# Kernel optimization log

Measured on AMD Instinct MI355X. Metric: run time of the kernel, lower is better.

## Reference

```python
import jax, jax.numpy as jnp
import numpy as np

N_QUBITS = 8
N_CYCLES = 4
N_LAYERS = 2  # log2(8) - 1
B = 65536

CNOT = jnp.array([[1, 0, 0, 0],
                  [0, 1, 0, 0],
                  [0, 0, 0, 1],
                  [0, 0, 1, 0]], dtype=jnp.complex64)


def apply_gate(state, U, wires):
    """Apply a (2^k x 2^k) gate U on the given wires of state (B, 2,2,...,2).
    Wire 0 is the leftmost (most significant) qubit axis."""
    k = len(wires)
    src = [w + 1 for w in wires]
    dst = list(range(1, 1 + k))
    st = jnp.moveaxis(state, src, dst)
    shp = st.shape
    st = st.reshape(shp[0], 2 ** k, -1)
    st = jnp.einsum('ij,bjr->bir', U, st)
    return jnp.moveaxis(st.reshape(shp), dst, src)


def apply_ry(state, q, angles):
    """Batched RY(angle) on qubit q; angles has shape (B,)."""
    st = jnp.moveaxis(state, q + 1, 1)  # (B, 2, rest...)
    c = jnp.cos(0.5 * angles).reshape((-1,) + (1,) * (st.ndim - 2))
    s = jnp.sin(0.5 * angles).reshape((-1,) + (1,) * (st.ndim - 2))
    s0, s1 = st[:, 0], st[:, 1]
    new = jnp.stack([c * s0 - s * s1, s * s0 + c * s1], axis=1)
    return jnp.moveaxis(new, 1, q + 1)


def crx_mat(theta):
    c = (jnp.cos(0.5 * theta) + 0j).astype(jnp.complex64)
    s = (-1j * jnp.sin(0.5 * theta)).astype(jnp.complex64)
    one = jnp.ones((), jnp.complex64)
    zero = jnp.zeros((), jnp.complex64)
    return jnp.stack([
        jnp.stack([one, zero, zero, zero]),
        jnp.stack([zero, one, zero, zero]),
        jnp.stack([zero, zero, c, s]),
        jnp.stack([zero, zero, s, c]),
    ])


def u3_mat(p):
    th, ph, lm = p[0], p[1], p[2]
    ct = (jnp.cos(0.5 * th) + 0j).astype(jnp.complex64)
    st = (jnp.sin(0.5 * th) + 0j).astype(jnp.complex64)
    el = jnp.exp(1j * lm).astype(jnp.complex64)
    ep = jnp.exp(1j * ph).astype(jnp.complex64)
    return jnp.stack([
        jnp.stack([ct, -el * st]),
        jnp.stack([ep * st, ep * el * ct]),
    ])


def expval_z(state, q):
    st = jnp.moveaxis(state, q + 1, 1)
    p = (st.real ** 2 + st.imag ** 2).reshape(st.shape[0], 2, -1).sum(-1)
    return p[:, 0] - p[:, 1]


def _forward(x, crx_theta, u3_params, w1, b1, w2, b2):
    b = x.shape[0]
    # |0...0> initial state, shape (B, 2,2,...,2)
    state = jnp.zeros((b, 2 ** N_QUBITS), jnp.complex64).at[:, 0].set(1.0)
    state = state.reshape((b,) + (2,) * N_QUBITS)
    # encoder: data re-uploading RY angle encoding + CNOT ring, n_cycles times
    for _ in range(N_CYCLES):
        for q in range(N_QUBITS):
            state = apply_ry(state, q, x[:, q])
        for q in range(N_QUBITS):
            state = apply_gate(state, CNOT, [q, (q + 1) % N_QUBITS])
    # QCNN conv/pool layers with shared weights per layer
    active = list(range(N_QUBITS))
    for layer in range(N_LAYERS):
        U = crx_mat(crx_theta[layer])
        for i in range(0, len(active) - 1, 2):
            state = apply_gate(state, U, [active[i], active[i + 1]])
        for i in range(1, len(active) - 1, 2):
            state = apply_gate(state, U, [active[i], active[i + 1]])
        remain = active[1::2]
        # mid-circuit expval in the original is discarded and does not alter state
        V = u3_mat(u3_params[layer])
        for q in remain:
            state = apply_gate(state, V, [q])
        active = remain
    feats = jnp.stack([expval_z(state, q) for q in active], axis=1)  # (B, 2)
    h = jnp.tanh(feats @ w1 + b1)
    return jax.nn.sigmoid(h @ w2 + b2)  # (B, 1)


def setup_inputs() -> dict:
    key = jax.random.key(0)
    ks = jax.random.split(key, 6)
    return {
        'x': jax.random.normal(ks[0], (B, N_QUBITS), jnp.float32),
        'crx_theta': jax.random.normal(ks[1], (N_LAYERS,), jnp.float32),
        'u3_params': jax.random.normal(ks[2], (N_LAYERS, 3), jnp.float32),
        'w1': jax.random.normal(ks[3], (2, 10), jnp.float32) * 0.5,
        'b1': jnp.zeros((10,), jnp.float32),
        'w2': jax.random.normal(ks[4], (10, 1), jnp.float32) * 0.5,
        'b2': jnp.zeros((1,), jnp.float32),
    }


def reference(x, crx_theta, u3_params, w1, b1, w2, b2):
    return _forward(x, crx_theta, u3_params, w1, b1, w2, b2)
```

## Files before the change

kernel.cpp:

```cpp
#include <hip/hip_runtime.h>


#define NQ 8
typedef _Float16 h2 __attribute__((ext_vector_type(2)));

__device__ __forceinline__ float h2f(h2 v){ return __builtin_bit_cast(float, v); }
__device__ __forceinline__ h2 f2h(float v){ return __builtin_bit_cast(h2, v); }
__device__ __forceinline__ h2 u2h(unsigned u){ return __builtin_bit_cast(h2, u); }
__device__ __forceinline__ h2 negh(h2 v){ return __builtin_bit_cast(h2, __builtin_bit_cast(unsigned, v) ^ 0x80008000u); }
__device__ __forceinline__ h2 mk(float x){ _Float16 h=(_Float16)x; return (h2){h,h}; }
__device__ __forceinline__ h2 mk2(float a, float b){ return (h2){(_Float16)a,(_Float16)b}; }
__device__ __forceinline__ h2 fma2h(h2 a, h2 b, h2 c){ return __builtin_elementwise_fma(a,b,c); }
__device__ __forceinline__ h2 swp(h2 v){ return __builtin_shufflevector(v,v,1,0); }

template<int CTRL>
__device__ __forceinline__ float dppf(float v){
    return __int_as_float(__builtin_amdgcn_mov_dpp(__float_as_int(v), CTRL, 0xF, 0xF, true));
}
template<int M>
__device__ __forceinline__ float sx(float v){
    if constexpr (M==1)       return dppf<0xB1>(v);
    else if constexpr (M==2)  return dppf<0x4E>(v);
    else if constexpr (M==8)  return dppf<0x128>(v);
    else if constexpr (M==32) return __shfl_xor(v, 32, 64);
    else return __int_as_float(__builtin_amdgcn_ds_swizzle(__float_as_int(v), (M<<10)|0x1F));
}
__device__ __forceinline__ float bperm(int ba, float v){
    return __int_as_float(__builtin_amdgcn_ds_bpermute(ba, __float_as_int(v)));
}
__device__ __forceinline__ void cmulh(h2&R, h2&I, h2 C, h2 S, h2 nS){
    h2 nR = fma2h(C, R, nS*I);
    I = fma2h(C, I, S*R);
    R = nR;
}

__global__ void qcnn_prep(const float* __restrict__ crx,
                          const float* __restrict__ u3p,
                          unsigned* __restrict__ ws){
    if (threadIdx.x==0 && blockIdx.x==0){
        auto PK=[](float lo, float hi)->unsigned{
            unsigned a=__builtin_bit_cast(unsigned short,(_Float16)lo);
            unsigned b=__builtin_bit_cast(unsigned short,(_Float16)hi);
            return a | (b<<16);
        };
        float sc0,cc0,sc1,cc1;
        __sincosf(0.5f*crx[0],&sc0,&cc0);
        __sincosf(0.5f*crx[1],&sc1,&cc1);
        ws[0]=PK(cc0,cc0); ws[1]=PK(sc0,sc0); ws[2]=PK(cc1,cc1); ws[3]=PK(sc1,sc1);
        float th0=u3p[0], ph0=u3p[1], lm0=u3p[2];
        float ust0,uct0; __sincosf(0.5f*th0,&ust0,&uct0);
        ws[4]=PK(uct0,uct0); ws[5]=PK(ust0,ust0); ws[6]=PK(-ust0,-ust0); ws[7]=PK(-ust0,ust0);
        float th1=u3p[3], ph1=u3p[4], lm1=u3p[5];
        float ust1,uct1; __sincosf(0.5f*th1,&ust1,&uct1);
        float sl1,cl1;   __sincosf(lm1,&sl1,&cl1);
        float sp1,cp1;   __sincosf(ph1,&sp1,&cp1);
        ws[8]=PK(uct1,uct1); ws[9]=PK(ust1,ust1); ws[10]=PK(-ust1,-ust1);
        ws[11]=PK(cl1,cl1); ws[12]=PK(sl1,sl1); ws[13]=PK(cp1,cp1); ws[14]=PK(sp1,sp1);
        float cpl1=cp1*cl1-sp1*sl1, spl1=sp1*cl1+cp1*sl1;
        float u01r=-ust1*cl1, u01i=-ust1*sl1;
        float u10r= ust1*cp1, u10i= ust1*sp1;
        float u11r= uct1*cpl1, u11i= uct1*spl1;
        ws[15]=PK(uct1,u11r); ws[16]=PK(u01r,u10r); ws[17]=PK(0.f,-u11i);
        ws[18]=PK(-u01i,-u10i); ws[19]=PK(0.f,u11i); ws[20]=PK(u01i,u10i);
        for(int k=0;k<4;++k){
            float kf=(float)k, sA,cA,sB,cB,sA2,cA2,sB2,cB2;
            __sincosf(lm0*kf,      &sA,&cA);
            __sincosf(lm0*(kf+1.f),&sB,&cB);
            __sincosf(ph0*kf,      &sA2,&cA2);
            __sincosf(ph0*(kf+1.f),&sB2,&cB2);
            unsigned* q = ws + 24 + k*4;
            q[0]=PK(cA,cB); q[1]=PK(sA,sB); q[2]=PK(cA2,cB2); q[3]=PK(sA2,sB2);
        }
    }
}

__global__ __launch_bounds__(256) void qcnn_kernel(
    const float* __restrict__ x,
    const unsigned* __restrict__ wsu,
    const float* __restrict__ w1,
    const float* __restrict__ b1,
    const float* __restrict__ w2,
    const float* __restrict__ b2,
    float* __restrict__ out,
    int Btot)
{
    const int gtid = blockIdx.x*256 + threadIdx.x;
    const int e = gtid >> 6;
    const int l = threadIdx.x & 63;
    if (e >= Btot) return;
    const bool L5=(l>>5)&1, L4=(l>>4)&1, L3=(l>>3)&1, L2=(l>>2)&1, L1=(l>>1)&1, L0=l&1;

    const bool pb = __builtin_popcount(l) & 1;
    const int ba0 = (((l&32)|((l^(l>>1))&31)) << 2);
    const int ba1 = ba0 ^ (48<<2);

    const float4* xv = (const float4*)(x + e*NQ);
    float4 xa=xv[0], xb=xv[1];
    float ang[8]={xa.x,xa.y,xa.z,xa.w,xb.x,xb.y,xb.z,xb.w};
    float cq[8], sq[8];
#pragma unroll
    for(int q=0;q<8;++q) __sincosf(0.5f*ang[q], &sq[q], &cq[q]);
    h2 cH[6], tsH[6];
    const bool bits[6]={L5,L4,L3,L2,L1,L0};
#pragma unroll
    for(int q=0;q<6;++q){
        cH[q]=mk(cq[q]);
        h2 sh=mk(sq[q]);
        tsH[q]= bits[q] ? sh : negh(sh);
    }
    h2 c6h=mk(cq[6]), s6h=mk(sq[6]), ns6h=negh(s6h);
    h2 c7h=mk(cq[7]), sv7h=mk2(-sq[7], sq[7]);

    const h2 cc0h=u2h(wsu[0]), sn0h=u2h(wsu[1]), cc1h=u2h(wsu[2]), sn1h=u2h(wsu[3]);
    const h2 nsn0h=negh(sn0h), nsn1h=negh(sn1h);
    const h2 uct0h=u2h(wsu[4]), ust0h=u2h(wsu[5]), nust0h=u2h(wsu[6]), usv0h=u2h(wsu[7]);
    const h2 uct1h=u2h(wsu[8]), ust1h=u2h(wsu[9]), nust1h=u2h(wsu[10]);
    const h2 cl1h=u2h(wsu[11]), sl1h=u2h(wsu[12]), nsl1h=negh(sl1h);
    const h2 cp1h=u2h(wsu[13]), sp1h=u2h(wsu[14]), nsp1h=negh(sp1h);
    const h2 E0h=u2h(wsu[15]), E1h=u2h(wsu[16]), E2h=u2h(wsu[17]);
    const h2 E3h=u2h(wsu[18]), G2h=u2h(wsu[19]), G3h=u2h(wsu[20]);
    const int ki = (int)L4 + (int)L2 + (int)L0;
    uint4 dt = *(const uint4*)(wsu + 24 + ki*4);
    const h2 Clm=u2h(dt.x), Slm=u2h(dt.y), Cph=u2h(dt.z), Sph=u2h(dt.w);
    const h2 nSlm=negh(Slm), nSph=negh(Sph);
    const h2 tu1H = L4 ? ust0h : nust0h;
    const h2 tu3H = L2 ? ust0h : nust0h;
    const h2 tu5H = L0 ? ust0h : nust0h;

    h2 A, B;
    {
        float pl = (L5?sq[0]:cq[0])*(L4?sq[1]:cq[1])*(L3?sq[2]:cq[2])
                 * (L2?sq[3]:cq[3])*(L1?sq[4]:cq[4])*(L0?sq[5]:cq[5]);
        float pc6=pl*cq[6], ps6=pl*sq[6];
        A = mk2(pc6*cq[7], pc6*sq[7]);
        B = mk2(ps6*cq[7], ps6*sq[7]);
    }

#define RY_L(q, M) do { \
    h2 oA = f2h(sx<M>(h2f(A))), oB = f2h(sx<M>(h2f(B))); \
    A = fma2h(cH[q], A, tsH[q]*oA); \
    B = fma2h(cH[q], B, tsH[q]*oB); \
} while(0)

#define RINGF() do { \
    float TA = h2f(pb ? B : A); \
    float TS = h2f(swp(pb ? A : B)); \
    float u0 = bperm(ba0, TA), u1 = bperm(ba1, TA); \
    float w0 = bperm(ba0, TS), w1 = bperm(ba1, TS); \
    A = (h2){ f2h(u0).x, f2h(u1).y }; \
    B = (h2){ f2h(w0).x, f2h(w1).y }; \
} while(0)

    RINGF();
#pragma unroll
    for(int cyc=0;cyc<3;++cyc){
        RY_L(0,32); RY_L(1,16); RY_L(2,8); RY_L(3,4); RY_L(4,2); RY_L(5,1);
        { h2 nA = fma2h(c6h, A, ns6h*B);
          h2 nB = fma2h(s6h, A, c6h*B);
          A=nA; B=nB; }
        A = fma2h(c7h, A, sv7h*swp(A));
        B = fma2h(c7h, B, sv7h*swp(B));
        RINGF();
    }

    h2 RA=A, RB=B, IA=(h2){0,0}, IB=(h2){0,0};

#define SHF4(M) h2 oRA=f2h(sx<M>(h2f(RA))), oIA=f2h(sx<M>(h2f(IA))), \
                   oRB=f2h(sx<M>(h2f(RB))), oIB=f2h(sx<M>(h2f(IB)));
#define CRX_LL(CSH, M, cc, sn, nsn) do { \
    const bool ct = (l >> (CSH)) & 1; \
    SHF4(M) \
    if (ct) { \
        RA = fma2h(cc, RA, (sn)*oIA); IA = fma2h(cc, IA, (nsn)*oRA); \
        RB = fma2h(cc, RB, (sn)*oIB); IB = fma2h(cc, IB, (nsn)*oRB); } \
} while(0)
#define RYC0(M, T) do { \
    SHF4(M) \
    RA = fma2h(uct0h, RA, (T)*oRA); IA = fma2h(uct0h, IA, (T)*oIA); \
    RB = fma2h(uct0h, RB, (T)*oRB); IB = fma2h(uct0h, IB, (T)*oIB); \
} while(0)

    {   h2 oA = f2h(sx<16>(h2f(RA))), oB = f2h(sx<16>(h2f(RB)));
        if (L5){ IA = nsn0h*oA; RA = cc0h*RA; IB = nsn0h*oB; RB = cc0h*RB; }
    }
    CRX_LL(3, 4, cc0h, sn0h, nsn0h);
    CRX_LL(1, 1, cc0h, sn0h, nsn0h);
    {   h2 oI = swp(IB), oR = swp(RB);
        RB = fma2h(cc0h, RB, sn0h*oI);
        IB = fma2h(cc0h, IB, nsn0h*oR);
    }
    CRX_LL(4, 8, cc0h, sn0h, nsn0h);
    CRX_LL(2, 2, cc0h, sn0h, nsn0h);
    if (L0) {
        h2 nRA = fma2h(cc0h, RA, sn0h*IB);
        h2 nRB = fma2h(cc0h, RB, sn0h*IA);
        h2 nIA = fma2h(cc0h, IA, nsn0h*RB);
        h2 nIB = fma2h(cc0h, IB, nsn0h*RA);
        RA=nRA; RB=nRB; IA=nIA; IB=nIB;
    }
    cmulh(RA,IA,Clm,Slm,nSlm); cmulh(RB,IB,Clm,Slm,nSlm);
    RYC0(16, tu1H);
    RYC0(4,  tu3H);
    RYC0(1,  tu5H);
    {   h2 sA=swp(RA), sB=swp(RB), tA=swp(IA), tB=swp(IB);
        RA = fma2h(uct0h, RA, usv0h*sA); RB = fma2h(uct0h, RB, usv0h*sB);
        IA = fma2h(uct0h, IA, usv0h*tA); IB = fma2h(uct0h, IB, usv0h*tB);
    }
    cmulh(RA,IA,Cph,Sph,nSph); cmulh(RB,IB,Cph,Sph,nSph);

    CRX_LL(4, 4, cc1h, sn1h, nsn1h);
    if (L0) {
        h2 sIA=swp(IA), sRA=swp(RA), sIB=swp(IB), sRB=swp(RB);
        RA = fma2h(cc1h, RA, sn1h*sIA); IA = fma2h(cc1h, IA, nsn1h*sRA);
        RB = fma2h(cc1h, RB, sn1h*sIB); IB = fma2h(cc1h, IB, nsn1h*sRB);
    }
    CRX_LL(2, 1, cc1h, sn1h, nsn1h);
    {
        if (L2){ cmulh(RA,IA,cl1h,sl1h,nsl1h); cmulh(RB,IB,cl1h,sl1h,nsl1h); }
        h2 T = L2 ? ust1h : nust1h;
        SHF4(4)
        RA = fma2h(uct1h, RA, T*oRA); IA = fma2h(uct1h, IA, T*oIA);
        RB = fma2h(uct1h, RB, T*oRB); IB = fma2h(uct1h, IB, T*oIB);
        if (L2){ cmulh(RA,IA,cp1h,sp1h,nsp1h); cmulh(RB,IB,cp1h,sp1h,nsp1h); }
    }
    {
        h2 sR=swp(RA), sI=swp(IA);
        h2 nR = fma2h(E3h,sI, fma2h(E2h,IA, fma2h(E1h,sR, E0h*RA)));
        h2 nI = fma2h(G3h,sR, fma2h(G2h,RA, fma2h(E1h,sI, E0h*IA)));
        RA=nR; IA=nI;
        h2 sR2=swp(RB), sI2=swp(IB);
        h2 nR2 = fma2h(E3h,sI2, fma2h(E2h,IB, fma2h(E1h,sR2, E0h*RB)));
        h2 nI2 = fma2h(G3h,sR2, fma2h(G2h,RB, fma2h(E1h,sI2, E0h*IB)));
        RB=nR2; IB=nI2;
    }

    float r0=(float)RA.x, r1=(float)RA.y, r2=(float)RB.x, r3=(float)RB.y;
    float i0=(float)IA.x, i1=(float)IA.y, i2=(float)IB.x, i3=(float)IB.y;
    float n0=fmaf(i0,i0,r0*r0), n1=fmaf(i1,i1,r1*r1);
    float n2=fmaf(i2,i2,r2*r2), n3=fmaf(i3,i3,r3*r3);
    float tot=(n0+n1)+(n2+n3);
    float f0 = L2 ? -tot : tot;
    float f1 = (n0-n1)+(n2-n3);
    f0 += sx<1>(f0);  f1 += sx<1>(f1);
    f0 += sx<2>(f0);  f1 += sx<2>(f1);
    f0 += sx<4>(f0);  f1 += sx<4>(f1);
    f0 += sx<8>(f0);  f1 += sx<8>(f1);
    f0 += sx<16>(f0); f1 += sx<16>(f1);
    f0 += sx<32>(f0); f1 += sx<32>(f1);

    const int k = l & 15;
    float contrib = 0.0f;
    if (k < 10) {
        float z = fmaf(f0, w1[k], fmaf(f1, w1[10+k], b1[k]));
        float ex = __expf(2.0f*z);
        contrib = ((ex-1.0f)/(ex+1.0f)) * w2[k];
    }
    contrib += sx<1>(contrib);
    contrib += sx<2>(contrib);
    contrib += sx<4>(contrib);
    contrib += sx<8>(contrib);
    if (l == 0) {
        float a = contrib + b2[0];
        out[e] = 1.0f/(1.0f + __expf(-a));
    }
}

extern "C" void kernel_launch(void* const* d_in, const int* in_sizes, int n_in,
                              void* d_out, int out_size, void* d_ws, size_t ws_size,
                              hipStream_t stream) {
    const float* x   = (const float*)d_in[0];
    const float* crx = (const float*)d_in[1];
    const float* u3p = (const float*)d_in[2];
    const float* w1  = (const float*)d_in[3];
    const float* b1  = (const float*)d_in[4];
    const float* w2  = (const float*)d_in[5];
    const float* b2  = (const float*)d_in[6];
    float* out = (float*)d_out;
    unsigned* ws = (unsigned*)d_ws;

    const int B = in_sizes[0] / NQ;
    hipLaunchKernelGGL(qcnn_prep, dim3(1), dim3(64), 0, stream, crx, u3p, ws);
    const int wavesPerBlock = 4;
    const int grid = (B + wavesPerBlock - 1) / wavesPerBlock;
    hipLaunchKernelGGL(qcnn_kernel, dim3(grid), dim3(256), 0, stream,
                       x, ws, w1, b1, w2, b2, out, B);
}
```

Baseline: 122.0 us.

## Process two batch elements per wavefront to amortize per-wave setup and add ILP

```diff
diff --git a/kernel.cpp b/kernel.cpp
--- a/kernel.cpp
+++ b/kernel.cpp
@@ -21,7 +21,6 @@
 __device__ __forceinline__ float sx(float v){
     if constexpr (M==1)       return dppf<0xB1>(v);
     else if constexpr (M==2)  return dppf<0x4E>(v);
-    else if constexpr (M==8)  return dppf<0x128>(v);
     else if constexpr (M==32) return __shfl_xor(v, 32, 64);
     else return __int_as_float(__builtin_amdgcn_ds_swizzle(__float_as_int(v), (M<<10)|0x1F));
 }
@@ -33,6 +32,8 @@
     I = fma2h(C, I, S*R);
     R = nR;
 }
+
+#define FOR_E _Pragma("unroll") for (int e = 0; e < 2; ++e)
 
 __global__ void qcnn_prep(const float* __restrict__ crx,
                           const float* __restrict__ u3p,
@@ -85,31 +86,41 @@
     int Btot)
 {
     const int gtid = blockIdx.x*256 + threadIdx.x;
-    const int e = gtid >> 6;
+    const int wv = gtid >> 6;
     const int l = threadIdx.x & 63;
-    if (e >= Btot) return;
+    const int e0 = wv * 2;
+    if (e0 >= Btot) return;
     const bool L5=(l>>5)&1, L4=(l>>4)&1, L3=(l>>3)&1, L2=(l>>2)&1, L1=(l>>1)&1, L0=l&1;
 
     const bool pb = __builtin_popcount(l) & 1;
     const int ba0 = (((l&32)|((l^(l>>1))&31)) << 2);
     const int ba1 = ba0 ^ (48<<2);
 
-    const float4* xv = (const float4*)(x + e*NQ);
-    float4 xa=xv[0], xb=xv[1];
-    float ang[8]={xa.x,xa.y,xa.z,xa.w,xb.x,xb.y,xb.z,xb.w};
-    float cq[8], sq[8];
+    h2 cH[2][6], tsH[2][6];
+    h2 c6h[2], s6h[2], ns6h[2], c7h[2], sv7h[2];
+    h2 A[2], B[2];
+    const bool bits[6]={L5,L4,L3,L2,L1,L0};
+    FOR_E {
+        const float4* xv = (const float4*)(x + (e0+e)*NQ);
+        float4 xa=xv[0], xb=xv[1];
+        float ang[8]={xa.x,xa.y,xa.z,xa.w,xb.x,xb.y,xb.z,xb.w};
+        float cq[8], sq[8];
 #pragma unroll
-    for(int q=0;q<8;++q) __sincosf(0.5f*ang[q], &sq[q], &cq[q]);
-    h2 cH[6], tsH[6];
-    const bool bits[6]={L5,L4,L3,L2,L1,L0};
+        for(int q=0;q<8;++q) __sincosf(0.5f*ang[q], &sq[q], &cq[q]);
 #pragma unroll
-    for(int q=0;q<6;++q){
-        cH[q]=mk(cq[q]);
-        h2 sh=mk(sq[q]);
-        tsH[q]= bits[q] ? sh : negh(sh);
-    }
-    h2 c6h=mk(cq[6]), s6h=mk(sq[6]), ns6h=negh(s6h);
-    h2 c7h=mk(cq[7]), sv7h=mk2(-sq[7], sq[7]);
+        for(int q=0;q<6;++q){
+            cH[e][q]=mk(cq[q]);
+            h2 sh=mk(sq[q]);
+            tsH[e][q]= bits[q] ? sh : negh(sh);
+        }
+        c6h[e]=mk(cq[6]); s6h[e]=mk(sq[6]); ns6h[e]=negh(s6h[e]);
+        c7h[e]=mk(cq[7]); sv7h[e]=mk2(-sq[7], sq[7]);
+        float pl = (L5?sq[0]:cq[0])*(L4?sq[1]:cq[1])*(L3?sq[2]:cq[2])
+                 * (L2?sq[3]:cq[3])*(L1?sq[4]:cq[4])*(L0?sq[5]:cq[5]);
+        float pc6=pl*cq[6], ps6=pl*sq[6];
+        A[e] = mk2(pc6*cq[7], pc6*sq[7]);
+        B[e] = mk2(ps6*cq[7], ps6*sq[7]);
+    }
 
     const h2 cc0h=u2h(wsu[0]), sn0h=u2h(wsu[1]), cc1h=u2h(wsu[2]), sn1h=u2h(wsu[3]);
     const h2 nsn0h=negh(sn0h), nsn1h=negh(sn1h);
@@ -127,131 +138,136 @@
     const h2 tu3H = L2 ? ust0h : nust0h;
     const h2 tu5H = L0 ? ust0h : nust0h;
 
-    h2 A, B;
-    {
-        float pl = (L5?sq[0]:cq[0])*(L4?sq[1]:cq[1])*(L3?sq[2]:cq[2])
-                 * (L2?sq[3]:cq[3])*(L1?sq[4]:cq[4])*(L0?sq[5]:cq[5]);
-        float pc6=pl*cq[6], ps6=pl*sq[6];
-        A = mk2(pc6*cq[7], pc6*sq[7]);
-        B = mk2(ps6*cq[7], ps6*sq[7]);
-    }
-
-#define RY_L(q, M) do { \
-    h2 oA = f2h(sx<M>(h2f(A))), oB = f2h(sx<M>(h2f(B))); \
-    A = fma2h(cH[q], A, tsH[q]*oA); \
-    B = fma2h(cH[q], B, tsH[q]*oB); \
+#define RY_L(q, M) do { FOR_E { \
+    h2 oA = f2h(sx<M>(h2f(A[e]))), oB = f2h(sx<M>(h2f(B[e]))); \
+    A[e] = fma2h(cH[e][q], A[e], tsH[e][q]*oA); \
+    B[e] = fma2h(cH[e][q], B[e], tsH[e][q]*oB); } \
 } while(0)
 
-#define RINGF() do { \
-    float TA = h2f(pb ? B : A); \
-    float TS = h2f(swp(pb ? A : B)); \
+#define RINGF() do { FOR_E { \
+    float TA = h2f(pb ? B[e] : A[e]); \
+    float TS = h2f(swp(pb ? A[e] : B[e])); \
     float u0 = bperm(ba0, TA), u1 = bperm(ba1, TA); \
     float w0 = bperm(ba0, TS), w1 = bperm(ba1, TS); \
-    A = (h2){ f2h(u0).x, f2h(u1).y }; \
-    B = (h2){ f2h(w0).x, f2h(w1).y }; \
+    A[e] = (h2){ f2h(u0).x, f2h(u1).y }; \
+    B[e] = (h2){ f2h(w0).x, f2h(w1).y }; } \
 } while(0)
 
     RINGF();
 #pragma unroll
     for(int cyc=0;cyc<3;++cyc){
         RY_L(0,32); RY_L(1,16); RY_L(2,8); RY_L(3,4); RY_L(4,2); RY_L(5,1);
-        { h2 nA = fma2h(c6h, A, ns6h*B);
-          h2 nB = fma2h(s6h, A, c6h*B);
-          A=nA; B=nB; }
-        A = fma2h(c7h, A, sv7h*swp(A));
-        B = fma2h(c7h, B, sv7h*swp(B));
+        FOR_E { h2 nA = fma2h(c6h[e], A[e], ns6h[e]*B[e]);
+                h2 nB = fma2h(s6h[e], A[e], c6h[e]*B[e]);
+                A[e]=nA; B[e]=nB; }
+        FOR_E { A[e] = fma2h(c7h[e], A[e], sv7h[e]*swp(A[e]));
+                B[e] = fma2h(c7h[e], B[e], sv7h[e]*swp(B[e])); }
         RINGF();
     }
 
-    h2 RA=A, RB=B, IA=(h2){0,0}, IB=(h2){0,0};
-
-#define SHF4(M) h2 oRA=f2h(sx<M>(h2f(RA))), oIA=f2h(sx<M>(h2f(IA))), \
-                   oRB=f2h(sx<M>(h2f(RB))), oIB=f2h(sx<M>(h2f(IB)));
+    h2 RA[2], RB[2], IA[2], IB[2];
+    FOR_E { RA[e]=A[e]; RB[e]=B[e]; IA[e]=(h2){0,0}; IB[e]=(h2){0,0}; }
+
+#define SHF4(M) h2 oRA[2], oIA[2], oRB[2], oIB[2]; \
+    FOR_E { oRA[e]=f2h(sx<M>(h2f(RA[e]))); oIA[e]=f2h(sx<M>(h2f(IA[e]))); \
+            oRB[e]=f2h(sx<M>(h2f(RB[e]))); oIB[e]=f2h(sx<M>(h2f(IB[e]))); }
 #define CRX_LL(CSH, M, cc, sn, nsn) do { \
     const bool ct = (l >> (CSH)) & 1; \
     SHF4(M) \
-    if (ct) { \
-        RA = fma2h(cc, RA, (sn)*oIA); IA = fma2h(cc, IA, (nsn)*oRA); \
-        RB = fma2h(cc, RB, (sn)*oIB); IB = fma2h(cc, IB, (nsn)*oRB); } \
+    if (ct) { FOR_E { \
+        RA[e] = fma2h(cc, RA[e], (sn)*oIA[e]); IA[e] = fma2h(cc, IA[e], (nsn)*oRA[e]); \
+        RB[e] = fma2h(cc, RB[e], (sn)*oIB[e]); IB[e] = fma2h(cc, IB[e], (nsn)*oRB[e]); } } \
 } while(0)
 #define RYC0(M, T) do { \
     SHF4(M) \
-    RA = fma2h(uct0h, RA, (T)*oRA); IA = fma2h(uct0h, IA, (T)*oIA); \
-    RB = fma2h(uct0h, RB, (T)*oRB); IB = fma2h(uct0h, IB, (T)*oIB); \
+    FOR_E { \
+    RA[e] = fma2h(uct0h, RA[e], (T)*oRA[e]); IA[e] = fma2h(uct0h, IA[e], (T)*oIA[e]); \
+    RB[e] = fma2h(uct0h, RB[e], (T)*oRB[e]); IB[e] = fma2h(uct0h, IB[e], (T)*oIB[e]); } \
 } while(0)
 
-    {   h2 oA = f2h(sx<16>(h2f(RA))), oB = f2h(sx<16>(h2f(RB)));
-        if (L5){ IA = nsn0h*oA; RA = cc0h*RA; IB = nsn0h*oB; RB = cc0h*RB; }
+    {   h2 oA[2], oB[2];
+        FOR_E { oA[e]=f2h(sx<16>(h2f(RA[e]))); oB[e]=f2h(sx<16>(h2f(RB[e]))); }
+        if (L5){ FOR_E {
+            IA[e] = nsn0h*oA[e]; RA[e] = cc0h*RA[e];
+            IB[e] = nsn0h*oB[e]; RB[e] = cc0h*RB[e]; } }
     }
     CRX_LL(3, 4, cc0h, sn0h, nsn0h);
     CRX_LL(1, 1, cc0h, sn0h, nsn0h);
-    {   h2 oI = swp(IB), oR = swp(RB);
-        RB = fma2h(cc0h, RB, sn0h*oI);
-        IB = fma2h(cc0h, IB, nsn0h*oR);
+    FOR_E {
+        h2 oI = swp(IB[e]), oR = swp(RB[e]);
+        RB[e] = fma2h(cc0h, RB[e], sn0h*oI);
+        IB[e] = fma2h(cc0h, IB[e], nsn0h*oR);
     }
     CRX_LL(4, 8, cc0h, sn0h, nsn0h);
     CRX_LL(2, 2, cc0h, sn0h, nsn0h);
-    if (L0) {
-        h2 nRA = fma2h(cc0h, RA, sn0h*IB);
-        h2 nRB = fma2h(cc0h, RB, sn0h*IA);
-        h2 nIA = fma2h(cc0h, IA, nsn0h*RB);
-        h2 nIB = fma2h(cc0h, IB, nsn0h*RA);
-        RA=nRA; RB=nRB; IA=nIA; IB=nIB;
-    }
-    cmulh(RA,IA,Clm,Slm,nSlm); cmulh(RB,IB,Clm,Slm,nSlm);
+    if (L0) { FOR_E {
+        h2 nRA = fma2h(cc0h, RA[e], sn0h*IB[e]);
+        h2 nRB = fma2h(cc0h, RB[e], sn0h*IA[e]);
+        h2 nIA = fma2h(cc0h, IA[e], nsn0h*RB[e]);
+        h2 nIB = fma2h(cc0h, IB[e], nsn0h*RA[e]);
+        RA[e]=nRA; RB[e]=nRB; IA[e]=nIA; IB[e]=nIB; } }
+    FOR_E { cmulh(RA[e],IA[e],Clm,Slm,nSlm); cmulh(RB[e],IB[e],Clm,Slm,nSlm); }
     RYC0(16, tu1H);
     RYC0(4,  tu3H);
     RYC0(1,  tu5H);
-    {   h2 sA=swp(RA), sB=swp(RB), tA=swp(IA), tB=swp(IB);
-        RA = fma2h(uct0h, RA, usv0h*sA); RB = fma2h(uct0h, RB, usv0h*sB);
-        IA = fma2h(uct0h, IA, usv0h*tA); IB = fma2h(uct0h, IB, usv0h*tB);
-    }
-    cmulh(RA,IA,Cph,Sph,nSph); cmulh(RB,IB,Cph,Sph,nSph);
+    FOR_E {
+        h2 sA=swp(RA[e]), sB=swp(RB[e]), tA=swp(IA[e]), tB=swp(IB[e]);
+        RA[e] = fma2h(uct0h, RA[e], usv0h*sA); RB[e] = fma2h(uct0h, RB[e], usv0h*sB);
+        IA[e] = fma2h(uct0h, IA[e], usv0h*tA); IB[e] = fma2h(uct0h, IB[e], usv0h*tB);
+    }
+    FOR_E { cmulh(RA[e],IA[e],Cph,Sph,nSph); cmulh(RB[e],IB[e],Cph,Sph,nSph); }
 
     CRX_LL(4, 4, cc1h, sn1h, nsn1h);
-    if (L0) {
-        h2 sIA=swp(IA), sRA=swp(RA), sIB=swp(IB), sRB=swp(RB);
-        RA = fma2h(cc1h, RA, sn1h*sIA); IA = fma2h(cc1h, IA, nsn1h*sRA);
-        RB = fma2h(cc1h, RB, sn1h*sIB); IB = fma2h(cc1h, IB, nsn1h*sRB);
-    }
+    if (L0) { FOR_E {
+        h2 sIA=swp(IA[e]), sRA=swp(RA[e]), sIB=swp(IB[e]), sRB=swp(RB[e]);
+        RA[e] = fma2h(cc1h, RA[e], sn1h*sIA); IA[e] = fma2h(cc1h, IA[e], nsn1h*sRA);
+        RB[e] = fma2h(cc1h, RB[e], sn1h*sIB); IB[e] = fma2h(cc1h, IB[e], nsn1h*sRB); } }
     CRX_LL(2, 1, cc1h, sn1h, nsn1h);
     {
-        if (L2){ cmulh(RA,IA,cl1h,sl1h,nsl1h); cmulh(RB,IB,cl1h,sl1h,nsl1h); }
+        if (L2){ FOR_E { cmulh(RA[e],IA[e],cl1h,sl1h,nsl1h); cmulh(RB[e],IB[e],cl1h,sl1h,nsl1h); } }
         h2 T = L2 ? ust1h : nust1h;
         SHF4(4)
-        RA = fma2h(uct1h, RA, T*oRA); IA = fma2h(uct1h, IA, T*oIA);
-        RB = fma2h(uct1h, RB, T*oRB); IB = fma2h(uct1h, IB, T*oIB);
-        if (L2){ cmulh(RA,IA,cp1h,sp1h,nsp1h); cmulh(RB,IB,cp1h,sp1h,nsp1h); }
-    }
-    {
-        h2 sR=swp(RA), sI=swp(IA);
-        h2 nR = fma2h(E3h,sI, fma2h(E2h,IA, fma2h(E1h,sR, E0h*RA)));
-        h2 nI = fma2h(G3h,sR, fma2h(G2h,RA, fma2h(E1h,sI, E0h*IA)));
-        RA=nR; IA=nI;
-        h2 sR2=swp(RB), sI2=swp(IB);
-        h2 nR2 = fma2h(E3h,sI2, fma2h(E2h,IB, fma2h(E1h,sR2, E0h*RB)));
-        h2 nI2 = fma2h(G3h,sR2, fma2h(G2h,RB, fma2h(E1h,sI2, E0h*IB)));
-        RB=nR2; IB=nI2;
-    }
-
-    float r0=(float)RA.x, r1=(float)RA.y, r2=(float)RB.x, r3=(float)RB.y;
-    float i0=(float)IA.x, i1=(float)IA.y, i2=(float)IB.x, i3=(float)IB.y;
-    float n0=fmaf(i0,i0,r0*r0), n1=fmaf(i1,i1,r1*r1);
-    float n2=fmaf(i2,i2,r2*r2), n3=fmaf(i3,i3,r3*r3);
-    float tot=(n0+n1)+(n2+n3);
-    float f0 = L2 ? -tot : tot;
-    float f1 = (n0-n1)+(n2-n3);
-    f0 += sx<1>(f0);  f1 += sx<1>(f1);
-    f0 += sx<2>(f0);  f1 += sx<2>(f1);
-    f0 += sx<4>(f0);  f1 += sx<4>(f1);
-    f0 += sx<8>(f0);  f1 += sx<8>(f1);
-    f0 += sx<16>(f0); f1 += sx<16>(f1);
-    f0 += sx<32>(f0); f1 += sx<32>(f1);
+        FOR_E {
+            RA[e] = fma2h(uct1h, RA[e], T*oRA[e]); IA[e] = fma2h(uct1h, IA[e], T*oIA[e]);
+            RB[e] = fma2h(uct1h, RB[e], T*oRB[e]); IB[e] = fma2h(uct1h, IB[e], T*oIB[e]);
+        }
+        if (L2){ FOR_E { cmulh(RA[e],IA[e],cp1h,sp1h,nsp1h); cmulh(RB[e],IB[e],cp1h,sp1h,nsp1h); } }
+    }
+    FOR_E {
+        h2 sR=swp(RA[e]), sI=swp(IA[e]);
+        h2 nR = fma2h(E3h,sI, fma2h(E2h,IA[e], fma2h(E1h,sR, E0h*RA[e])));
+        h2 nI = fma2h(G3h,sR, fma2h(G2h,RA[e], fma2h(E1h,sI, E0h*IA[e])));
+        RA[e]=nR; IA[e]=nI;
+        h2 sR2=swp(RB[e]), sI2=swp(IB[e]);
+        h2 nR2 = fma2h(E3h,sI2, fma2h(E2h,IB[e], fma2h(E1h,sR2, E0h*RB[e])));
+        h2 nI2 = fma2h(G3h,sR2, fma2h(G2h,RB[e], fma2h(E1h,sI2, E0h*IB[e])));
+        RB[e]=nR2; IB[e]=nI2;
+    }
+
+    float f0[2], f1[2];
+    FOR_E {
+        float r0=(float)RA[e].x, r1=(float)RA[e].y, r2=(float)RB[e].x, r3=(float)RB[e].y;
+        float i0=(float)IA[e].x, i1=(float)IA[e].y, i2=(float)IB[e].x, i3=(float)IB[e].y;
+        float n0=fmaf(i0,i0,r0*r0), n1=fmaf(i1,i1,r1*r1);
+        float n2=fmaf(i2,i2,r2*r2), n3=fmaf(i3,i3,r3*r3);
+        float tot=(n0+n1)+(n2+n3);
+        f0[e] = L2 ? -tot : tot;
+        f1[e] = (n0-n1)+(n2-n3);
+    }
+    FOR_E { f0[e] += sx<1>(f0[e]);  f1[e] += sx<1>(f1[e]);  }
+    FOR_E { f0[e] += sx<2>(f0[e]);  f1[e] += sx<2>(f1[e]);  }
+    FOR_E { f0[e] += sx<4>(f0[e]);  f1[e] += sx<4>(f1[e]);  }
+    FOR_E { f0[e] += sx<8>(f0[e]);  f1[e] += sx<8>(f1[e]);  }
+    FOR_E { f0[e] += sx<16>(f0[e]); f1[e] += sx<16>(f1[e]); }
+    FOR_E { f0[e] += sx<32>(f0[e]); f1[e] += sx<32>(f1[e]); }
 
     const int k = l & 15;
+    const int row = l >> 4;
+    const float Fx = (row & 1) ? f0[1] : f0[0];
+    const float Fy = (row & 1) ? f1[1] : f1[0];
     float contrib = 0.0f;
     if (k < 10) {
-        float z = fmaf(f0, w1[k], fmaf(f1, w1[10+k], b1[k]));
+        float z = fmaf(Fx, w1[k], fmaf(Fy, w1[10+k], b1[k]));
         float ex = __expf(2.0f*z);
         contrib = ((ex-1.0f)/(ex+1.0f)) * w2[k];
     }
@@ -259,9 +275,9 @@
     contrib += sx<2>(contrib);
     contrib += sx<4>(contrib);
     contrib += sx<8>(contrib);
-    if (l == 0) {
+    if (k == 0 && row < 2) {
         float a = contrib + b2[0];
-        out[e] = 1.0f/(1.0f + __expf(-a));
+        out[e0 + row] = 1.0f/(1.0f + __expf(-a));
     }
 }
 
@@ -280,8 +296,9 @@
 
     const int B = in_sizes[0] / NQ;
     hipLaunchKernelGGL(qcnn_prep, dim3(1), dim3(64), 0, stream, crx, u3p, ws);
+    const int waves = (B + 1) / 2;
     const int wavesPerBlock = 4;
-    const int grid = (B + wavesPerBlock - 1) / wavesPerBlock;
+    const int grid = (waves + wavesPerBlock - 1) / wavesPerBlock;
     hipLaunchKernelGGL(qcnn_kernel, dim3(grid), dim3(256), 0, stream,
                        x, ws, w1, b1, w2, b2, out, B);
 }
```

New measurement: 119.7 us (median of 2 runs). About the same (-1.9%).
